# Kernel tuning notes

Hardware: AMD Instinct MI355X
Metric: run time of the kernel (lower is better)

Reference implementation:

```python
import jax, jax.numpy as jnp
import numpy as np
import math

HIDDEN = 1024
N_HEADS = 16
HEAD = HIDDEN // N_HEADS

def setup_inputs() -> dict:
    key = jax.random.key(0)
    k1, k2, k3 = jax.random.split(key, 3)
    encodings = jax.random.normal(k1, (2, 2048, HIDDEN), dtype=jnp.float32)
    W_attn = jax.random.normal(k2, (HIDDEN, 3 * HIDDEN), dtype=jnp.float32) * 0.02
    b_attn = jnp.zeros((3 * HIDDEN,), dtype=jnp.float32)
    W_out = jax.random.normal(k3, (HIDDEN, HIDDEN), dtype=jnp.float32) * 0.02
    b_out = jnp.zeros((HIDDEN,), dtype=jnp.float32)
    return {"encodings": encodings, "W_attn": W_attn, "b_attn": b_attn,
            "W_out": W_out, "b_out": b_out}

def reference(encodings, W_attn, b_attn, W_out, b_out):
    b, n, _ = encodings.shape
    qkv = encodings @ W_attn + b_attn              # [b, n, 3*hidden]
    q, k, v = jnp.split(qkv, 3, axis=-1)
    # 'b n (h l) -> b h n l'
    def to_heads(t):
        return t.reshape(b, n, N_HEADS, HEAD).transpose(0, 2, 1, 3)
    q, k, v = to_heads(q), to_heads(k), to_heads(v)
    # scores[b,h,k,q]; causal mask keeps key_pos <= query_pos
    scores = jnp.einsum('bhki,bhqi->bhkq', k, q) / math.sqrt(HEAD)
    mask = jnp.arange(n)[:, None] <= jnp.arange(n)[None, :]   # [k, q]
    scores = jnp.where(mask, scores, jnp.float32(-10000.0))
    attn = jax.nn.softmax(scores, axis=2)          # softmax over key dim
    combined = jnp.einsum('bhkq,bhkl->bhql', attn, v)  # [b, h, n, head]
    out = combined.transpose(0, 2, 1, 3).reshape(b, n, HIDDEN)
    return out @ W_out + b_out
```

## Files before the change

kernel.cpp:

```cpp
#include <hip/hip_runtime.h>
#include <hip/hip_bf16.h>

typedef __attribute__((ext_vector_type(8))) short bf16x8;
typedef __attribute__((ext_vector_type(4))) short bf16x4;
typedef __attribute__((ext_vector_type(4))) float f32x4;

__device__ __forceinline__ short f2bf(float f) {
    unsigned u = __float_as_uint(f);
    u += 0x7fff + ((u >> 16) & 1);
    return (short)(u >> 16);
}
__device__ __forceinline__ float bf2f(short s) {
    return __uint_as_float(((unsigned)(unsigned short)s) << 16);
}
__device__ __forceinline__ unsigned pk_bf16(float lo, float hi) {
    __hip_bfloat162 t = __float22bfloat162_rn(make_float2(lo, hi));
    unsigned u;
    __builtin_memcpy(&u, &t, 4);
    return u;
}

#define GLOAD_LDS16(gp, lp)                                                            \
    __builtin_amdgcn_global_load_lds(                                                  \
        (const __attribute__((address_space(1))) unsigned*)(gp),                       \
        (__attribute__((address_space(3))) unsigned*)(lp), 16, 0, 0)

#define QK_SCALE 0.180336879f
#define MFMA16(a, b, c) __builtin_amdgcn_mfma_f32_16x16x32_bf16((a), (b), (c), 0, 0, 0)

__device__ __forceinline__ void tcvt_tile(const float* __restrict__ W, short* __restrict__ Wt,
                                          int K, int N, int bx, int by, int t,
                                          short (*tile)[72]) {
    const int k0 = by * 64, n0 = bx * 64;
    #pragma unroll
    for (int jj = 0; jj < 4; ++jj) {
        int row = jj * 16 + (t >> 4);
        int col = (t & 15) * 4;
        f32x4 v = *(const f32x4*)&W[(size_t)(k0 + row) * N + n0 + col];
        bf16x4 b = {f2bf(v.x), f2bf(v.y), f2bf(v.z), f2bf(v.w)};
        *(bf16x4*)&tile[row][col] = b;
    }
    __syncthreads();
    const int nr = t >> 2, kc = (t & 3) * 16;
    bf16x8 o0, o1;
    #pragma unroll
    for (int j = 0; j < 8; ++j) { o0[j] = tile[kc + j][nr]; o1[j] = tile[kc + 8 + j][nr]; }
    short* dst = &Wt[(size_t)(n0 + nr) * K + k0 + kc];
    *(bf16x8*)dst = o0;
    *(bf16x8*)(dst + 8) = o1;
}

__global__ __launch_bounds__(256) void prep_kernel(
    const float* __restrict__ enc, const float* __restrict__ Wa,
    const float* __restrict__ ba, const float* __restrict__ Wo,
    const float* __restrict__ bo, short* __restrict__ Abf,
    short* __restrict__ WtA, short* __restrict__ bbA,
    short* __restrict__ WtO, short* __restrict__ bbO)
{
    __shared__ alignas(16) short tile[64][72];
    const int id = blockIdx.x, t = threadIdx.x;
    if (id < 2048) {
        const int i = id * 2048 + t * 8;
        f32x4 a = *(const f32x4*)&enc[i];
        f32x4 b = *(const f32x4*)&enc[i + 4];
        bf16x8 o = {f2bf(a.x), f2bf(a.y), f2bf(a.z), f2bf(a.w),
                    f2bf(b.x), f2bf(b.y), f2bf(b.z), f2bf(b.w)};
        *(bf16x8*)&Abf[i] = o;
    } else if (id == 2048) {
        for (int j = t * 8; j < 3072; j += 2048) {
            f32x4 a = *(const f32x4*)&ba[j];
            f32x4 b = *(const f32x4*)&ba[j + 4];
            bf16x8 o = {f2bf(a.x), f2bf(a.y), f2bf(a.z), f2bf(a.w),
                        f2bf(b.x), f2bf(b.y), f2bf(b.z), f2bf(b.w)};
            *(bf16x8*)&bbA[j] = o;
        }
    } else if (id == 2049) {
        if (t < 128) {
            const int j = t * 8;
            f32x4 a = *(const f32x4*)&bo[j];
            f32x4 b = *(const f32x4*)&bo[j + 4];
            bf16x8 o = {f2bf(a.x), f2bf(a.y), f2bf(a.z), f2bf(a.w),
                        f2bf(b.x), f2bf(b.y), f2bf(b.z), f2bf(b.w)};
            *(bf16x8*)&bbO[j] = o;
        }
        __syncthreads();
    } else if (id < 2818) {
        const int lid = id - 2050;
        tcvt_tile(Wa, WtA, 1024, 3072, lid % 48, lid / 48, t, tile);
    } else {
        const int lid = id - 2818;
        tcvt_tile(Wo, WtO, 1024, 1024, lid % 16, lid / 16, t, tile);
    }
}

template<int BN, bool F32OUT, bool SPLIT3>
__global__ __launch_bounds__(256) void gemm_bt(
    const short* __restrict__ A, const short* __restrict__ Bt,
    const short* __restrict__ bias, void* __restrict__ C,
    short* __restrict__ Kw, short* __restrict__ Vw, int M, int N, int K)
{
    __shared__ alignas(16) short As[128 * 32];
    __shared__ alignas(16) short Bs[BN * 32];

    const int tid = threadIdx.x, w = tid >> 6, lane = tid & 63;
    const int quad = lane >> 4, l16 = lane & 15;
    constexpr int MT = (BN == 128) ? 4 : 2;
    const int wm = (BN == 128) ? (w >> 1) : w;
    const int wn = (BN == 128) ? (w & 1) : 0;
    const int m0 = blockIdx.y * 128, n0 = blockIdx.x * BN;
    const int srow = lane >> 2, scol = (lane & 3) * 8;

    f32x4 acc[MT][4] = {};

    for (int k0 = 0; k0 < K; k0 += 32) {
        __syncthreads();
        #pragma unroll
        for (int jj = 0; jj < 2; ++jj) {
            const int rb = w * 32 + jj * 16;
            GLOAD_LDS16(&A[(size_t)(m0 + rb + srow) * K + k0 + scol], &As[rb * 32]);
        }
        if (BN == 128) {
            #pragma unroll
            for (int jj = 0; jj < 2; ++jj) {
                const int rb = w * 32 + jj * 16;
                GLOAD_LDS16(&Bt[(size_t)(n0 + rb + srow) * K + k0 + scol], &Bs[rb * 32]);
            }
        } else {
            const int rb = w * 16;
            GLOAD_LDS16(&Bt[(size_t)(n0 + rb + srow) * K + k0 + scol], &Bs[rb * 32]);
        }
        __syncthreads();
        bf16x8 af[MT], bfr[4];
        #pragma unroll
        for (int i = 0; i < MT; ++i)
            af[i] = *(const bf16x8*)&As[(wm * (MT * 16) + i * 16 + l16) * 32 + quad * 8];
        #pragma unroll
        for (int i = 0; i < 4; ++i)
            bfr[i] = *(const bf16x8*)&Bs[(wn * 64 + i * 16 + l16) * 32 + quad * 8];
        #pragma unroll
        for (int mt = 0; mt < MT; ++mt)
            #pragma unroll
            for (int nt = 0; nt < 4; ++nt)
                acc[mt][nt] = MFMA16(af[mt], bfr[nt], acc[mt][nt]);
    }

    if (SPLIT3) {
        const int g = n0 >> 10;
        short* dstb = (g == 0) ? (short*)C : (g == 1) ? Kw : Vw;
        const int lc0 = n0 & 1023;
        #pragma unroll
        for (int nt = 0; nt < 4; ++nt) {
            const int col = n0 + wn * 64 + nt * 16 + l16;
            const int lc = lc0 + wn * 64 + nt * 16 + l16;
            const float bv = bf2f(bias[col]);
            #pragma unroll
            for (int mt = 0; mt < 4; ++mt) {
                const int row = m0 + wm * 64 + mt * 16 + quad * 4;
                #pragma unroll
                for (int r = 0; r < 4; ++r) {
                    float v = acc[mt][nt][r] + bv;
                    if (g == 0) v *= QK_SCALE;
                    dstb[(size_t)(row + r) * 1024 + lc] = f2bf(v);
                }
            }
        }
    } else {
        #pragma unroll
        for (int nt = 0; nt < 4; ++nt) {
            const int col = n0 + wn * 64 + nt * 16 + l16;
            const float bv = bf2f(bias[col]);
            #pragma unroll
            for (int mt = 0; mt < MT; ++mt) {
                const int row = m0 + wm * (MT * 16) + mt * 16 + quad * 4;
                #pragma unroll
                for (int r = 0; r < 4; ++r) {
                    float v = acc[mt][nt][r] + bv;
                    if (F32OUT) ((float*)C)[(size_t)(row + r) * N + col] = v;
                    else        ((short*)C)[(size_t)(row + r) * N + col] = f2bf(v);
                }
            }
        }
    }
}

__global__ __launch_bounds__(256) void fragprep_kernel(
    const short* __restrict__ Kw, const short* __restrict__ Vw,
    short* __restrict__ Kx, short* __restrict__ Vx)
{
    __shared__ alignas(16) short T[64][72];
    const int t = threadIdx.x;
    const int kc = blockIdx.x, bh = blockIdx.y;
    const int batch = bh >> 4, head = bh & 15;
    const size_t srcbase = ((size_t)batch * 2048 + kc * 64) * 1024 + head * 64;
    short* kxdst = Kx + ((size_t)bh * 32 + kc) * 4096;
    short* vxdst = Vx + ((size_t)bh * 32 + kc) * 4096;

    #pragma unroll
    for (int i = 0; i < 2; ++i) {
        const int c = i * 256 + t;
        const int lane = c & 63, sh = c >> 6;
        const int s = sh >> 1, h = sh & 1;
        const int l16 = lane & 15, quad = lane >> 4;
        bf16x8 v = *(const bf16x8*)&Kw[srcbase + (size_t)(s * 16 + l16) * 1024 + h * 32 + quad * 8];
        *(bf16x8*)&kxdst[c * 8] = v;
    }
    #pragma unroll
    for (int i = 0; i < 2; ++i) {
        const int c = i * 256 + t;
        const int row = c >> 3, d0 = (c & 7) * 8;
        bf16x8 v = *(const bf16x8*)&Vw[srcbase + (size_t)row * 1024 + d0];
        #pragma unroll
        for (int j = 0; j < 8; ++j) T[d0 + j][row] = v[j];
    }
    __syncthreads();
    #pragma unroll
    for (int i = 0; i < 2; ++i) {
        const int c = i * 256 + t;
        const int lane = c & 63, hd = c >> 6;
        const int h = hd >> 2, dt = hd & 3;
        const int l16 = lane & 15, quad = lane >> 4;
        bf16x8 v = *(const bf16x8*)&T[dt * 16 + l16][h * 32 + quad * 8];
        *(bf16x8*)&vxdst[c * 8] = v;
    }
}

__global__ __launch_bounds__(128) void attn_kernel(
    const short* __restrict__ Qw, const short* __restrict__ Kx,
    const short* __restrict__ Vx, short* __restrict__ comb)
{
    __shared__ alignas(16) short Ps[2][2][16 * 72];

    const int tid = threadIdx.x, w = tid >> 6, lane = tid & 63;
    const int quad = lane >> 4, l16 = lane & 15;
    const int bh = blockIdx.x;
    const int tA = blockIdx.y, tB = 63 - tA;
    const int batch = bh >> 4, head = bh & 15;
    const size_t rowbase = (size_t)batch * 2048;
    const int hcol = head * 64;
    const int q0A = tA * 32 + w * 16, q0B = tB * 32 + w * 16;
    const int diagA = tA >> 1, diagB = tB >> 1;
    const short* Kxbh = Kx + (size_t)bh * 131072;
    const short* Vxbh = Vx + (size_t)bh * 131072;
    const int lofs = lane * 8;
    short* pwA = &Ps[w][0][0];
    short* pwB = &Ps[w][1][0];

    bf16x8 qfA[2], qfB[2];
    {
        const short* pa = &Qw[(rowbase + q0A + l16) * 1024 + hcol];
        const short* pb = &Qw[(rowbase + q0B + l16) * 1024 + hcol];
        qfA[0] = *(const bf16x8*)(pa + quad * 8);
        qfA[1] = *(const bf16x8*)(pa + 32 + quad * 8);
        qfB[0] = *(const bf16x8*)(pb + quad * 8);
        qfB[1] = *(const bf16x8*)(pb + 32 + quad * 8);
    }

    f32x4 otA[4] = {}, otB[4] = {};
    float laccA = 0.f, laccB = 0.f;

    bf16x8 kf[4][2];
    #pragma unroll
    for (int s = 0; s < 4; ++s) {
        kf[s][0] = *(const bf16x8*)&Kxbh[(s * 2 + 0) * 512 + lofs];
        kf[s][1] = *(const bf16x8*)&Kxbh[(s * 2 + 1) * 512 + lofs];
    }

    for (int kc = 0; kc <= diagB; ++kc) {
        const bool actA = (kc <= diagA);
        const int key0 = kc * 64;

        const short* vb = Vxbh + kc * 4096;
        bf16x8 vf[2][4];
        #pragma unroll
        for (int h = 0; h < 2; ++h)
            #pragma unroll
            for (int dt = 0; dt < 4; ++dt)
                vf[h][dt] = *(const bf16x8*)&vb[(h * 4 + dt) * 512 + lofs];

        f32x4 svA[4], svB[4];
        #pragma unroll
        for (int s = 0; s < 4; ++s) {
            f32x4 a = {0.f, 0.f, 0.f, 0.f};
            a = MFMA16(kf[s][0], qfB[0], a);
            a = MFMA16(kf[s][1], qfB[1], a);
            svB[s] = a;
            if (actA) {
                f32x4 b = {0.f, 0.f, 0.f, 0.f};
                b = MFMA16(kf[s][0], qfA[0], b);
                b = MFMA16(kf[s][1], qfA[1], b);
                svA[s] = b;
            }
        }

        if (kc < diagB) {
            const short* kb = Kxbh + (kc + 1) * 4096;
            #pragma unroll
            for (int s = 0; s < 4; ++s) {
                kf[s][0] = *(const bf16x8*)&kb[(s * 2 + 0) * 512 + lofs];
                kf[s][1] = *(const bf16x8*)&kb[(s * 2 + 1) * 512 + lofs];
            }
        }

        if (kc == diagB) {
            const int qq = q0B + l16;
            #pragma unroll
            for (int s = 0; s < 4; ++s) {
                const int keyb = key0 + s * 16 + quad * 4;
                #pragma unroll
                for (int r = 0; r < 4; ++r)
                    svB[s][r] = (keyb + r <= qq) ? svB[s][r] : -1e30f;
            }
        }
        #pragma unroll
        for (int s = 0; s < 4; ++s) {
            #pragma unroll
            for (int r = 0; r < 4; ++r) svB[s][r] = exp2f(svB[s][r]);
            laccB += (svB[s][0] + svB[s][1]) + (svB[s][2] + svB[s][3]);
            *(unsigned*)&pwB[l16 * 72 + s * 16 + quad * 4]     = pk_bf16(svB[s][0], svB[s][1]);
            *(unsigned*)&pwB[l16 * 72 + s * 16 + quad * 4 + 2] = pk_bf16(svB[s][2], svB[s][3]);
        }
        if (actA) {
            if (kc == diagA) {
                const int qq = q0A + l16;
                #pragma unroll
                for (int s = 0; s < 4; ++s) {
                    const int keyb = key0 + s * 16 + quad * 4;
                    #pragma unroll
                    for (int r = 0; r < 4; ++r)
                        svA[s][r] = (keyb + r <= qq) ? svA[s][r] : -1e30f;
                }
            }
            #pragma unroll
            for (int s = 0; s < 4; ++s) {
                #pragma unroll
                for (int r = 0; r < 4; ++r) svA[s][r] = exp2f(svA[s][r]);
                laccA += (svA[s][0] + svA[s][1]) + (svA[s][2] + svA[s][3]);
                *(unsigned*)&pwA[l16 * 72 + s * 16 + quad * 4]     = pk_bf16(svA[s][0], svA[s][1]);
                *(unsigned*)&pwA[l16 * 72 + s * 16 + quad * 4 + 2] = pk_bf16(svA[s][2], svA[s][3]);
            }
        }

        {
            bf16x8 pfB0 = *(const bf16x8*)&pwB[l16 * 72 + quad * 8];
            bf16x8 pfB1 = *(const bf16x8*)&pwB[l16 * 72 + 32 + quad * 8];
            #pragma unroll
            for (int dt = 0; dt < 4; ++dt) {
                otB[dt] = MFMA16(vf[0][dt], pfB0, otB[dt]);
                otB[dt] = MFMA16(vf[1][dt], pfB1, otB[dt]);
            }
            if (actA) {
                bf16x8 pfA0 = *(const bf16x8*)&pwA[l16 * 72 + quad * 8];
                bf16x8 pfA1 = *(const bf16x8*)&pwA[l16 * 72 + 32 + quad * 8];
                #pragma unroll
                for (int dt = 0; dt < 4; ++dt) {
                    otA[dt] = MFMA16(vf[0][dt], pfA0, otA[dt]);
                    otA[dt] = MFMA16(vf[1][dt], pfA1, otA[dt]);
                }
            }
        }
    }

    laccA += __shfl_xor(laccA, 16);
    laccA += __shfl_xor(laccA, 32);
    laccB += __shfl_xor(laccB, 16);
    laccB += __shfl_xor(laccB, 32);
    const float invA = 1.0f / laccA, invB = 1.0f / laccB;

    #pragma unroll
    for (int dt = 0; dt < 4; ++dt) {
        *(unsigned*)&pwA[l16 * 72 + dt * 16 + quad * 4]     = pk_bf16(otA[dt][0] * invA, otA[dt][1] * invA);
        *(unsigned*)&pwA[l16 * 72 + dt * 16 + quad * 4 + 2] = pk_bf16(otA[dt][2] * invA, otA[dt][3] * invA);
        *(unsigned*)&pwB[l16 * 72 + dt * 16 + quad * 4]     = pk_bf16(otB[dt][0] * invB, otB[dt][1] * invB);
        *(unsigned*)&pwB[l16 * 72 + dt * 16 + quad * 4 + 2] = pk_bf16(otB[dt][2] * invB, otB[dt][3] * invB);
    }
    {
        const int qr = lane >> 2, dc = (lane & 3) * 16;
        bf16x8 a0 = *(const bf16x8*)&pwA[qr * 72 + dc];
        bf16x8 a1 = *(const bf16x8*)&pwA[qr * 72 + dc + 8];
        short* dstA = &comb[(rowbase + q0A + qr) * 1024 + hcol + dc];
        *(bf16x8*)dstA = a0;
        *(bf16x8*)(dstA + 8) = a1;
        bf16x8 b0 = *(const bf16x8*)&pwB[qr * 72 + dc];
        bf16x8 b1 = *(const bf16x8*)&pwB[qr * 72 + dc + 8];
        short* dstB = &comb[(rowbase + q0B + qr) * 1024 + hcol + dc];
        *(bf16x8*)dstB = b0;
        *(bf16x8*)(dstB + 8) = b1;
    }
}

extern "C" void kernel_launch(void* const* d_in, const int* in_sizes, int n_in,
                              void* d_out, int out_size, void* d_ws, size_t ws_size,
                              hipStream_t stream)
{
    const float* enc = (const float*)d_in[0];
    const float* Wa  = (const float*)d_in[1];
    const float* ba  = (const float*)d_in[2];
    const float* Wo  = (const float*)d_in[3];
    const float* bo  = (const float*)d_in[4];
    float* out = (float*)d_out;

    char* ws = (char*)d_ws;
    short* Abf  = (short*)ws;
    short* Kx   = (short*)ws;
    short* WtO  = (short*)(ws + ((size_t)8 << 20));
    short* bbA  = (short*)(ws + ((size_t)10 << 20));
    short* bbO  = (short*)(ws + ((size_t)10 << 20) + 16384);
    short* WtA  = (short*)(ws + ((size_t)11 << 20));
    short* Vx   = (short*)(ws + ((size_t)11 << 20));
    short* Qw   = (short*)(ws + ((size_t)19 << 20));
    short* Kw   = (short*)(ws + ((size_t)27 << 20));
    short* comb = (short*)(ws + ((size_t)27 << 20));
    short* Vw   = (short*)(ws + ((size_t)35 << 20));

    prep_kernel<<<3074, 256, 0, stream>>>(enc, Wa, ba, Wo, bo, Abf, WtA, bbA, WtO, bbO);
    gemm_bt<128, false, true><<<dim3(24, 32), 256, 0, stream>>>(
        Abf, WtA, bbA, Qw, Kw, Vw, 4096, 3072, 1024);
    fragprep_kernel<<<dim3(32, 32), 256, 0, stream>>>(Kw, Vw, Kx, Vx);
    attn_kernel<<<dim3(32, 32), 128, 0, stream>>>(Qw, Kx, Vx, comb);
    gemm_bt<64, true, false><<<dim3(16, 32), 256, 0, stream>>>(
        comb, WtO, bbO, out, nullptr, nullptr, 4096, 1024, 1024);
}
```

Before: 190.5 us.

## Split attention key loop across two wave pairs and reduce partials in LDS

Doubles the attention block to four waves, with each pair processing alternating 64-key chunks for the same query tiles. Partial output accumulators and row sums from the second pair are written to shared memory and added by the first pair before normalisation and store. This targets the low wave count and long serial key loop per block, at the cost of extra LDS, two barriers, and a reduction epilogue.

```diff
diff --git a/kernel.cpp b/kernel.cpp
--- a/kernel.cpp
+++ b/kernel.cpp
@@ -224,13 +224,17 @@
     }
 }
 
-__global__ __launch_bounds__(128) void attn_kernel(
+__global__ __launch_bounds__(256) void attn_kernel(
     const short* __restrict__ Qw, const short* __restrict__ Kx,
     const short* __restrict__ Vx, short* __restrict__ comb)
 {
-    __shared__ alignas(16) short Ps[2][2][16 * 72];
-
-    const int tid = threadIdx.x, w = tid >> 6, lane = tid & 63;
+    __shared__ alignas(16) short Ps[4][2][16 * 72];
+    __shared__ alignas(16) float cbuf[2][2][64][16];
+    __shared__ float clacc[2][2][64];
+
+    const int tid = threadIdx.x, w4 = tid >> 6, lane = tid & 63;
+    const int w = w4 & 1;
+    const int h = w4 >> 1;
     const int quad = lane >> 4, l16 = lane & 15;
     const int bh = blockIdx.x;
     const int tA = blockIdx.y, tB = 63 - tA;
@@ -242,8 +246,8 @@
     const short* Kxbh = Kx + (size_t)bh * 131072;
     const short* Vxbh = Vx + (size_t)bh * 131072;
     const int lofs = lane * 8;
-    short* pwA = &Ps[w][0][0];
-    short* pwB = &Ps[w][1][0];
+    short* pwA = &Ps[w4][0][0];
+    short* pwB = &Ps[w4][1][0];
 
     bf16x8 qfA[2], qfB[2];
     {
@@ -259,23 +263,26 @@
     float laccA = 0.f, laccB = 0.f;
 
     bf16x8 kf[4][2];
-    #pragma unroll
-    for (int s = 0; s < 4; ++s) {
-        kf[s][0] = *(const bf16x8*)&Kxbh[(s * 2 + 0) * 512 + lofs];
-        kf[s][1] = *(const bf16x8*)&Kxbh[(s * 2 + 1) * 512 + lofs];
-    }
-
-    for (int kc = 0; kc <= diagB; ++kc) {
+    {
+        const short* kb0 = Kxbh + (size_t)h * 4096;
+        #pragma unroll
+        for (int s = 0; s < 4; ++s) {
+            kf[s][0] = *(const bf16x8*)&kb0[(s * 2 + 0) * 512 + lofs];
+            kf[s][1] = *(const bf16x8*)&kb0[(s * 2 + 1) * 512 + lofs];
+        }
+    }
+
+    for (int kc = h; kc <= diagB; kc += 2) {
         const bool actA = (kc <= diagA);
         const int key0 = kc * 64;
 
-        const short* vb = Vxbh + kc * 4096;
+        const short* vb = Vxbh + (size_t)kc * 4096;
         bf16x8 vf[2][4];
         #pragma unroll
-        for (int h = 0; h < 2; ++h)
+        for (int hh = 0; hh < 2; ++hh)
             #pragma unroll
             for (int dt = 0; dt < 4; ++dt)
-                vf[h][dt] = *(const bf16x8*)&vb[(h * 4 + dt) * 512 + lofs];
+                vf[hh][dt] = *(const bf16x8*)&vb[(hh * 4 + dt) * 512 + lofs];
 
         f32x4 svA[4], svB[4];
         #pragma unroll
@@ -292,8 +299,8 @@
             }
         }
 
-        if (kc < diagB) {
-            const short* kb = Kxbh + (kc + 1) * 4096;
+        if (kc + 2 <= diagB) {
+            const short* kb = Kxbh + (size_t)(kc + 2) * 4096;
             #pragma unroll
             for (int s = 0; s < 4; ++s) {
                 kf[s][0] = *(const bf16x8*)&kb[(s * 2 + 0) * 512 + lofs];
@@ -360,31 +367,52 @@
         }
     }
 
-    laccA += __shfl_xor(laccA, 16);
-    laccA += __shfl_xor(laccA, 32);
-    laccB += __shfl_xor(laccB, 16);
-    laccB += __shfl_xor(laccB, 32);
-    const float invA = 1.0f / laccA, invB = 1.0f / laccB;
-
-    #pragma unroll
-    for (int dt = 0; dt < 4; ++dt) {
-        *(unsigned*)&pwA[l16 * 72 + dt * 16 + quad * 4]     = pk_bf16(otA[dt][0] * invA, otA[dt][1] * invA);
-        *(unsigned*)&pwA[l16 * 72 + dt * 16 + quad * 4 + 2] = pk_bf16(otA[dt][2] * invA, otA[dt][3] * invA);
-        *(unsigned*)&pwB[l16 * 72 + dt * 16 + quad * 4]     = pk_bf16(otB[dt][0] * invB, otB[dt][1] * invB);
-        *(unsigned*)&pwB[l16 * 72 + dt * 16 + quad * 4 + 2] = pk_bf16(otB[dt][2] * invB, otB[dt][3] * invB);
-    }
-    {
-        const int qr = lane >> 2, dc = (lane & 3) * 16;
-        bf16x8 a0 = *(const bf16x8*)&pwA[qr * 72 + dc];
-        bf16x8 a1 = *(const bf16x8*)&pwA[qr * 72 + dc + 8];
-        short* dstA = &comb[(rowbase + q0A + qr) * 1024 + hcol + dc];
-        *(bf16x8*)dstA = a0;
-        *(bf16x8*)(dstA + 8) = a1;
-        bf16x8 b0 = *(const bf16x8*)&pwB[qr * 72 + dc];
-        bf16x8 b1 = *(const bf16x8*)&pwB[qr * 72 + dc + 8];
-        short* dstB = &comb[(rowbase + q0B + qr) * 1024 + hcol + dc];
-        *(bf16x8*)dstB = b0;
-        *(bf16x8*)(dstB + 8) = b1;
+    __syncthreads();
+    if (h == 1) {
+        #pragma unroll
+        for (int dt = 0; dt < 4; ++dt) {
+            *(f32x4*)&cbuf[w][0][lane][dt * 4] = otA[dt];
+            *(f32x4*)&cbuf[w][1][lane][dt * 4] = otB[dt];
+        }
+        clacc[w][0][lane] = laccA;
+        clacc[w][1][lane] = laccB;
+    }
+    __syncthreads();
+    if (h == 0) {
+        #pragma unroll
+        for (int dt = 0; dt < 4; ++dt) {
+            otA[dt] += *(const f32x4*)&cbuf[w][0][lane][dt * 4];
+            otB[dt] += *(const f32x4*)&cbuf[w][1][lane][dt * 4];
+        }
+        laccA += clacc[w][0][lane];
+        laccB += clacc[w][1][lane];
+
+        laccA += __shfl_xor(laccA, 16);
+        laccA += __shfl_xor(laccA, 32);
+        laccB += __shfl_xor(laccB, 16);
+        laccB += __shfl_xor(laccB, 32);
+        const float invA = 1.0f / laccA, invB = 1.0f / laccB;
+
+        #pragma unroll
+        for (int dt = 0; dt < 4; ++dt) {
+            *(unsigned*)&pwA[l16 * 72 + dt * 16 + quad * 4]     = pk_bf16(otA[dt][0] * invA, otA[dt][1] * invA);
+            *(unsigned*)&pwA[l16 * 72 + dt * 16 + quad * 4 + 2] = pk_bf16(otA[dt][2] * invA, otA[dt][3] * invA);
+            *(unsigned*)&pwB[l16 * 72 + dt * 16 + quad * 4]     = pk_bf16(otB[dt][0] * invB, otB[dt][1] * invB);
+            *(unsigned*)&pwB[l16 * 72 + dt * 16 + quad * 4 + 2] = pk_bf16(otB[dt][2] * invB, otB[dt][3] * invB);
+        }
+        {
+            const int qr = lane >> 2, dc = (lane & 3) * 16;
+            bf16x8 a0 = *(const bf16x8*)&pwA[qr * 72 + dc];
+            bf16x8 a1 = *(const bf16x8*)&pwA[qr * 72 + dc + 8];
+            short* dstA = &comb[(rowbase + q0A + qr) * 1024 + hcol + dc];
+            *(bf16x8*)dstA = a0;
+            *(bf16x8*)(dstA + 8) = a1;
+            bf16x8 b0 = *(const bf16x8*)&pwB[qr * 72 + dc];
+            bf16x8 b1 = *(const bf16x8*)&pwB[qr * 72 + dc + 8];
+            short* dstB = &comb[(rowbase + q0B + qr) * 1024 + hcol + dc];
+            *(bf16x8*)dstB = b0;
+            *(bf16x8*)(dstB + 8) = b1;
+        }
     }
 }
 
@@ -416,7 +444,7 @@
     gemm_bt<128, false, true><<<dim3(24, 32), 256, 0, stream>>>(
         Abf, WtA, bbA, Qw, Kw, Vw, 4096, 3072, 1024);
     fragprep_kernel<<<dim3(32, 32), 256, 0, stream>>>(Kw, Vw, Kx, Vx);
-    attn_kernel<<<dim3(32, 32), 128, 0, stream>>>(Qw, Kx, Vx, comb);
+    attn_kernel<<<dim3(32, 32), 256, 0, stream>>>(Qw, Kx, Vx, comb);
     gemm_bt<64, true, false><<<dim3(16, 32), 256, 0, stream>>>(
         comb, WtO, bbO, out, nullptr, nullptr, 4096, 1024, 1024);
 }
```

Measured after the change: 194.7 us. +2.2%, slower.
